# Kernel tuning notes

Hardware: AMD Instinct MI355X
Metric: run time of the kernel (lower is better)

## Reference

```python
import jax, jax.numpy as jnp
import numpy as np

N_MELS = 80
FORMANT_START, FORMANT_END = 10, 50
W_L1, W_DELTA, W_DELTA2, W_SC, W_BAND, FORMANT_W = 1.0, 0.5, 0.25, 0.5, 1.0, 2.0
EPS = 1e-8


def _masked_mean(x, mask):
    # mask broadcasts to x's shape; count = sum of the broadcast mask
    n = jnp.maximum(jnp.sum(jnp.broadcast_to(mask, x.shape)), 1.0)
    return jnp.sum(x * mask) / n


def setup_inputs() -> dict:
    key = jax.random.key(0)
    k1, k2, k3 = jax.random.split(key, 3)
    B, T, D = 64, 4000, N_MELS
    pred_mel = jax.random.normal(k1, (B, T, D), dtype=jnp.float32)
    target_mel = jax.random.normal(k2, (B, T, D), dtype=jnp.float32)
    lengths = jax.random.randint(k3, (B,), T // 2, T + 1)
    mel_mask = (jnp.arange(T)[None, :] < lengths[:, None]).astype(jnp.float32)
    band_weights = jnp.ones((D,), dtype=jnp.float32).at[FORMANT_START:FORMANT_END].set(FORMANT_W)
    return {"pred_mel": pred_mel, "target_mel": target_mel, "mel_mask": mel_mask,
            "band_weights": band_weights}


def reference(pred_mel, target_mel, mel_mask, band_weights):
    mask3 = mel_mask[:, :, None]                      # (B,T,1)

    l1 = jnp.abs(pred_mel - target_mel)               # (B,T,D)
    l1_loss = _masked_mean(l1, mask3)

    # 1st-order deltas
    dp = pred_mel[:, 1:] - pred_mel[:, :-1]
    dt = target_mel[:, 1:] - target_mel[:, :-1]
    dmask = (mel_mask[:, 1:] * mel_mask[:, :-1])[:, :, None]
    delta_loss = _masked_mean(jnp.abs(dp - dt), dmask)

    # 2nd-order deltas
    d2p = dp[:, 1:] - dp[:, :-1]
    d2t = dt[:, 1:] - dt[:, :-1]
    d2mask = (mel_mask[:, 2:] * mel_mask[:, 1:-1] * mel_mask[:, :-2])[:, :, None]
    delta2_loss = _masked_mean(jnp.abs(d2p - d2t), d2mask)

    # spectral convergence
    diff = (pred_mel - target_mel) * mask3
    tgt_m = target_mel * mask3
    n = jnp.maximum(jnp.sum(jnp.broadcast_to(mask3, pred_mel.shape)), 1.0)
    sc_num = jnp.sqrt(jnp.sum(diff * diff) / n)
    sc_den = jnp.maximum(jnp.sqrt(jnp.sum(tgt_m * tgt_m) / n), EPS)
    sc_loss = sc_num / sc_den

    # band-weighted L1
    w = band_weights[None, None, :]
    band_loss = _masked_mean(l1 * w, mask3) / jnp.mean(band_weights)

    # energy (per-frame mean over mel bins)
    e_l1 = jnp.abs(pred_mel.mean(axis=-1) - target_mel.mean(axis=-1))  # (B,T)
    energy_loss = _masked_mean(e_l1, mel_mask)

    return (W_L1 * l1_loss + W_DELTA * delta_loss + W_DELTA2 * delta2_loss
            + W_SC * sc_loss + W_BAND * band_loss + 0.5 * energy_loss)
```

## Files before the change

kernel.cpp:

```cpp
#include <hip/hip_runtime.h>
#include <math.h>

#define D_MELS 80
#define F4ROW  20
#define T_DIM  4000
#define NQM    7
#define NTHR   256
#define RPI    14

__global__ __launch_bounds__(NTHR) void mel_flags(
    const float* __restrict__ mask, int* __restrict__ bflag,
    float* __restrict__ cpart, int BT, int nmb, int rowsPerMB, int nfb)
{
    const int tid  = threadIdx.x;
    const int lane = tid & 63;
    const int wv   = tid >> 6;
    const int g    = blockIdx.x * (NTHR / 64) + wv;

    float cm = 0.f, cdm = 0.f, cd2m = 0.f;
    int   fl = 0;

    if (g < nmb) {
        const int rlo = g * rowsPerMB;
        int rhi = rlo + rowsPerMB; if (rhi > BT) rhi = BT;
        for (int r = rlo - 2 + lane; r < rhi; r += 64) {
            if (r < 0) continue;
            float m = mask[r];
            fl |= (m != 0.f);
            if (r >= rlo && m != 0.f) {
                int t = r % T_DIM;
                cm += m;
                if (t >= 1) {
                    float m1 = mask[r - 1];
                    cdm += m * m1;
                    if (t >= 2) cd2m += m * m1 * mask[r - 2];
                }
            }
        }
    }

    const bool anyl = __any(fl != 0);
    #pragma unroll
    for (int off = 32; off > 0; off >>= 1) {
        cm   += __shfl_down(cm,   off, 64);
        cdm  += __shfl_down(cdm,  off, 64);
        cd2m += __shfl_down(cd2m, off, 64);
    }
    if (g < nmb && lane == 0) bflag[g] = anyl ? 1 : 0;

    __shared__ float cred[NTHR / 64][3];
    if (lane == 0) { cred[wv][0] = cm; cred[wv][1] = cdm; cred[wv][2] = cd2m; }
    __syncthreads();
    if (tid < 3) {
        float s = 0.f;
        #pragma unroll
        for (int w2 = 0; w2 < NTHR / 64; ++w2) s += cred[w2][tid];
        cpart[tid * nfb + blockIdx.x] = s;
    }
}

__global__ __launch_bounds__(NTHR, 4) void mel_loss_main(
    const float* __restrict__ pred, const float* __restrict__ tgt,
    const float* __restrict__ mask, const int* __restrict__ bflag,
    float* __restrict__ partial, int BT, int Jtot, int K, int nmb)
{
    const int tid = threadIdx.x;

    if (!bflag[blockIdx.x]) {
        if (tid < NQM) partial[tid * nmb + blockIdx.x] = 0.f;
        return;
    }

    const int lane = tid & 63;
    const int qtr  = lane & 3;
    const int rw   = lane >> 2;
    const int wv   = tid >> 6;
    const int gw   = blockIdx.x * (NTHR / 64) + wv;

    const float4* p4 = (const float4*)pred;
    const float4* q4 = (const float4*)tgt;
    const int lsrc4 = (lane - 4) & 63;
    const int lsrc8 = (lane - 8) & 63;

    float v_l1 = 0.f, v_frr = 0.f, v_diff2 = 0.f, v_tgt2 = 0.f, v_energy = 0.f;
    float v_d = 0.f, v_d2 = 0.f;

    const int j0 = gw * K;
    for (int s = 0; s < K; ++s) {
        const int j = j0 + s;
        if (j >= Jtot) break;
        const int r = j * RPI - 2 + rw;
        const int rload = r < 0 ? 0 : (r >= BT ? BT - 1 : r);

        const size_t rowb = (size_t)rload * F4ROW + qtr;
        float  mload = mask[rload];
        float4 P[5], Q[5];
        #pragma unroll
        for (int k = 0; k < 5; ++k) P[k] = p4[rowb + 4 * k];
        #pragma unroll
        for (int k = 0; k < 5; ++k) Q[k] = q4[rowb + 4 * k];

        if (!__any(mload != 0.0f)) continue;

        const int t = rload % T_DIM;
        const float m1 = __shfl(mload, lsrc4, 64);
        const float m2 = __shfl(mload, lsrc8, 64);
        const bool contrib = (rw >= 2) && (r < BT);
        const float mt   = contrib ? mload : 0.f;
        const float dmv  = (t >= 1) ? mt * m1 : 0.f;
        const float d2mv = (t >= 2) ? dmv * m2 : 0.f;

        float l1r = 0.f, frr = 0.f, sqr = 0.f, t2r = 0.f, er = 0.f, dr = 0.f, d2r = 0.f;
        #pragma unroll
        for (int k = 0; k < 5; ++k) {
            float e0 = P[k].x - Q[k].x, e1 = P[k].y - Q[k].y,
                  e2 = P[k].z - Q[k].z, e3 = P[k].w - Q[k].w;

            float f0 = __shfl(e0, lsrc4, 64);
            float f1 = __shfl(e1, lsrc4, 64);
            float f2 = __shfl(e2, lsrc4, 64);
            float f3 = __shfl(e3, lsrc4, 64);
            float g0 = __shfl(e0, lsrc8, 64);
            float g1 = __shfl(e1, lsrc8, 64);
            float g2 = __shfl(e2, lsrc8, 64);
            float g3 = __shfl(e3, lsrc8, 64);

            float a0 = fabsf(e0), a1 = fabsf(e1), a2 = fabsf(e2), a3 = fabsf(e3);
            l1r += a0 + a1 + a2 + a3;
            const int d0 = (k << 4) + (qtr << 2);
            frr += ((unsigned)(d0 + 0 - 10) < 40u ? a0 : 0.f)
                 + ((unsigned)(d0 + 1 - 10) < 40u ? a1 : 0.f)
                 + ((unsigned)(d0 + 2 - 10) < 40u ? a2 : 0.f)
                 + ((unsigned)(d0 + 3 - 10) < 40u ? a3 : 0.f);
            sqr += e0 * e0 + e1 * e1 + e2 * e2 + e3 * e3;
            t2r += Q[k].x * Q[k].x + Q[k].y * Q[k].y + Q[k].z * Q[k].z + Q[k].w * Q[k].w;
            er  += e0 + e1 + e2 + e3;
            dr  += fabsf(e0 - f0) + fabsf(e1 - f1) + fabsf(e2 - f2) + fabsf(e3 - f3);
            d2r += fabsf(e0 - 2.f * f0 + g0) + fabsf(e1 - 2.f * f1 + g1)
                 + fabsf(e2 - 2.f * f2 + g2) + fabsf(e3 - 2.f * f3 + g3);
        }

        v_l1    += l1r * mt;
        v_frr   += frr * mt;
        v_diff2 += sqr * mt;
        v_tgt2  += t2r * mt;
        v_d     += dr * dmv;
        v_d2    += d2r * d2mv;

        er += __shfl_xor(er, 1, 64);
        er += __shfl_xor(er, 2, 64);
        if (qtr == 0) v_energy += fabsf(er) * mt;
    }

    float vals[NQM] = {v_l1, v_frr, v_diff2, v_tgt2, v_energy, v_d, v_d2};
    #pragma unroll
    for (int q = 0; q < NQM; ++q) {
        float v = vals[q];
        #pragma unroll
        for (int off = 32; off > 0; off >>= 1)
            v += __shfl_down(v, off, 64);
        vals[q] = v;
    }
    __shared__ float red[NTHR / 64][NQM];
    if (lane == 0) {
        #pragma unroll
        for (int q = 0; q < NQM; ++q) red[wv][q] = vals[q];
    }
    __syncthreads();
    if (tid < NQM) {
        float s = 0.f;
        #pragma unroll
        for (int w2 = 0; w2 < NTHR / 64; ++w2) s += red[w2][tid];
        partial[tid * nmb + blockIdx.x] = s;
    }
}

__global__ __launch_bounds__(640) void mel_loss_finalize(
    const float* __restrict__ partial, const float* __restrict__ cpart,
    const float* __restrict__ w, float* __restrict__ out, int nmb, int nfb)
{
    const int tid = threadIdx.x;
    const int wv  = tid >> 6;
    const int lane = tid & 63;
    __shared__ float fin[10];

    float s = 0.f;
    if (wv < NQM) {
        for (int i = lane; i < nmb; i += 64) s += partial[wv * nmb + i];
    } else {
        for (int i = lane; i < nfb; i += 64) s += cpart[(wv - NQM) * nfb + i];
    }
    #pragma unroll
    for (int off = 32; off > 0; off >>= 1) s += __shfl_down(s, off, 64);
    if (lane == 0 && wv < 10) fin[wv] = s;
    __syncthreads();

    if (tid == 0) {
        float l1s = fin[0], frrs = fin[1], diff2 = fin[2], tgt2 = fin[3];
        float energys = fin[4], ds = fin[5], d2s = fin[6];
        float ms = fin[7], dms = fin[8], d2ms = fin[9];

        float wsum = 0.f;
        for (int d = 0; d < D_MELS; ++d) wsum += w[d];
        float wmean = wsum / (float)D_MELS;

        float n1  = fmaxf(ms   * (float)D_MELS, 1.f);
        float nd  = fmaxf(dms  * (float)D_MELS, 1.f);
        float nd2 = fmaxf(d2ms * (float)D_MELS, 1.f);

        float l1_loss     = l1s / n1;
        float delta_loss  = ds / nd;
        float delta2_loss = d2s / nd2;
        float sc_num = sqrtf(diff2 / n1);
        float sc_den = fmaxf(sqrtf(tgt2 / n1), 1e-8f);
        float sc_loss = sc_num / sc_den;
        float band_loss = ((l1s + frrs) / n1) / wmean;
        float energy_loss = (energys / (float)D_MELS) / fmaxf(ms, 1.f);

        out[0] = 1.0f * l1_loss + 0.5f * delta_loss + 0.25f * delta2_loss
               + 0.5f * sc_loss + 1.0f * band_loss + 0.5f * energy_loss;
    }
}

extern "C" void kernel_launch(void* const* d_in, const int* in_sizes, int n_in,
                              void* d_out, int out_size, void* d_ws, size_t ws_size,
                              hipStream_t stream) {
    const float* pred = (const float*)d_in[0];
    const float* tgt  = (const float*)d_in[1];
    const float* mask = (const float*)d_in[2];
    const float* w    = (const float*)d_in[3];
    int BT = in_sizes[2];

    int Jtot = (BT + RPI - 1) / RPI;

    int K, nmb, nfb;
    size_t need;
    for (K = 1;; K *= 2) {
        int nwaves = (Jtot + K - 1) / K;
        nmb = (nwaves + (NTHR / 64) - 1) / (NTHR / 64);
        nfb = (nmb + (NTHR / 64) - 1) / (NTHR / 64);
        need = (size_t)(NQM * nmb + 3 * nfb) * sizeof(float) + (size_t)nmb * sizeof(int);
        if (need <= ws_size || K >= Jtot) break;
    }
    const int rowsPerMB = (NTHR / 64) * K * RPI;

    float* partial = (float*)d_ws;
    float* cpart   = partial + NQM * nmb;
    int*   bflag   = (int*)(cpart + 3 * nfb);

    mel_flags<<<nfb, NTHR, 0, stream>>>(mask, bflag, cpart, BT, nmb, rowsPerMB, nfb);
    mel_loss_main<<<nmb, NTHR, 0, stream>>>(pred, tgt, mask, bflag, partial, BT, Jtot, K, nmb);
    mel_loss_finalize<<<1, 640, 0, stream>>>(partial, cpart, w, (float*)d_out, nmb, nfb);
}
```

Measured before the change: 200.8 us.

## Remap lanes to DPP rows and replace shuffles with DPP row shifts

Lanes are remapped so that the 16 consecutive time rows of a tile share one DPP row, with the float4 column index taken from the high lane bits. The neighbour-row exchanges for the first and second deltas and for the mask then use DPP row_shr instead of LDS-backed shuffles, and the final wave reductions use DPP row shifts before two cross-row xor shuffles. The aim is to cut the cost of the many shuffle instructions in the inner loop. In exchange, each load instruction now reads strided rows instead of contiguous 64B runs, which may weaken coalescing. The minimum rows-per-wave factor K is also raised to 2.

Result: faster. 193.1 us (-3.9%).

```diff
diff --git a/kernel.cpp b/kernel.cpp
--- a/kernel.cpp
+++ b/kernel.cpp
@@ -7,6 +7,28 @@
 #define NQM    7
 #define NTHR   256
 #define RPI    14
+
+template<int CTRL>
+__device__ __forceinline__ float dppf(float v) {
+    return __int_as_float(__builtin_amdgcn_update_dpp(
+        0, __float_as_int(v), CTRL, 0xF, 0xF, true));
+}
+#define ROW_SHL1 0x101
+#define ROW_SHL2 0x102
+#define ROW_SHL4 0x104
+#define ROW_SHL8 0x108
+#define ROW_SHR1 0x111
+#define ROW_SHR2 0x112
+
+__device__ __forceinline__ float wave_sum(float v) {
+    v += dppf<ROW_SHL8>(v);
+    v += dppf<ROW_SHL4>(v);
+    v += dppf<ROW_SHL2>(v);
+    v += dppf<ROW_SHL1>(v);
+    v += __shfl_xor(v, 16, 64);
+    v += __shfl_xor(v, 32, 64);
+    return v;
+}
 
 __global__ __launch_bounds__(NTHR) void mel_flags(
     const float* __restrict__ mask, int* __restrict__ bflag,
@@ -72,15 +94,13 @@
     }
 
     const int lane = tid & 63;
-    const int qtr  = lane & 3;
-    const int rw   = lane >> 2;
+    const int qtr  = lane >> 4;
+    const int rw   = lane & 15;
     const int wv   = tid >> 6;
     const int gw   = blockIdx.x * (NTHR / 64) + wv;
 
     const float4* p4 = (const float4*)pred;
     const float4* q4 = (const float4*)tgt;
-    const int lsrc4 = (lane - 4) & 63;
-    const int lsrc8 = (lane - 8) & 63;
 
     float v_l1 = 0.f, v_frr = 0.f, v_diff2 = 0.f, v_tgt2 = 0.f, v_energy = 0.f;
     float v_d = 0.f, v_d2 = 0.f;
@@ -103,8 +123,8 @@
         if (!__any(mload != 0.0f)) continue;
 
         const int t = rload % T_DIM;
-        const float m1 = __shfl(mload, lsrc4, 64);
-        const float m2 = __shfl(mload, lsrc8, 64);
+        const float m1 = dppf<ROW_SHR1>(mload);
+        const float m2 = dppf<ROW_SHR2>(mload);
         const bool contrib = (rw >= 2) && (r < BT);
         const float mt   = contrib ? mload : 0.f;
         const float dmv  = (t >= 1) ? mt * m1 : 0.f;
@@ -116,14 +136,10 @@
             float e0 = P[k].x - Q[k].x, e1 = P[k].y - Q[k].y,
                   e2 = P[k].z - Q[k].z, e3 = P[k].w - Q[k].w;
 
-            float f0 = __shfl(e0, lsrc4, 64);
-            float f1 = __shfl(e1, lsrc4, 64);
-            float f2 = __shfl(e2, lsrc4, 64);
-            float f3 = __shfl(e3, lsrc4, 64);
-            float g0 = __shfl(e0, lsrc8, 64);
-            float g1 = __shfl(e1, lsrc8, 64);
-            float g2 = __shfl(e2, lsrc8, 64);
-            float g3 = __shfl(e3, lsrc8, 64);
+            float f0 = dppf<ROW_SHR1>(e0), f1 = dppf<ROW_SHR1>(e1),
+                  f2 = dppf<ROW_SHR1>(e2), f3 = dppf<ROW_SHR1>(e3);
+            float g0 = dppf<ROW_SHR2>(e0), g1 = dppf<ROW_SHR2>(e1),
+                  g2 = dppf<ROW_SHR2>(e2), g3 = dppf<ROW_SHR2>(e3);
 
             float a0 = fabsf(e0), a1 = fabsf(e1), a2 = fabsf(e2), a3 = fabsf(e3);
             l1r += a0 + a1 + a2 + a3;
@@ -147,20 +163,15 @@
         v_d     += dr * dmv;
         v_d2    += d2r * d2mv;
 
-        er += __shfl_xor(er, 1, 64);
-        er += __shfl_xor(er, 2, 64);
+        er += __shfl_xor(er, 16, 64);
+        er += __shfl_xor(er, 32, 64);
         if (qtr == 0) v_energy += fabsf(er) * mt;
     }
 
     float vals[NQM] = {v_l1, v_frr, v_diff2, v_tgt2, v_energy, v_d, v_d2};
     #pragma unroll
-    for (int q = 0; q < NQM; ++q) {
-        float v = vals[q];
-        #pragma unroll
-        for (int off = 32; off > 0; off >>= 1)
-            v += __shfl_down(v, off, 64);
-        vals[q] = v;
-    }
+    for (int q = 0; q < NQM; ++q) vals[q] = wave_sum(vals[q]);
+
     __shared__ float red[NTHR / 64][NQM];
     if (lane == 0) {
         #pragma unroll
@@ -235,7 +246,7 @@
 
     int K, nmb, nfb;
     size_t need;
-    for (K = 1;; K *= 2) {
+    for (K = 2;; K *= 2) {
         int nwaves = (Jtot + K - 1) / K;
         nmb = (nwaves + (NTHR / 64) - 1) / (NTHR / 64);
         nfb = (nmb + (NTHR / 64) - 1) / (NTHR / 64);
```
